# Performance work log

Hardware: AMD Instinct MI355X
Metric: run time of the kernel (lower is better)

## Reference

```python
import jax, jax.numpy as jnp
import numpy as np

DIM = 1024
HEADS = 16
DHEAD = 64
INNER = HEADS * DHEAD
EPS = 1e-5


def layer_norm(x, g, b):
    mu = jnp.mean(x, axis=-1, keepdims=True)
    var = jnp.mean(jnp.square(x - mu), axis=-1, keepdims=True)
    return (x - mu) * jax.lax.rsqrt(var + EPS) * g + b


def apply_rope(x, cos, sin):
    # x: [b, h, s, d]; cos/sin broadcast as [1, 1, s, d/2]
    d2 = x.shape[-1] // 2
    x1, x2 = x[..., :d2], x[..., d2:]
    return jnp.concatenate([x1 * cos - x2 * sin, x2 * cos + x1 * sin], axis=-1)


def setup_inputs() -> dict:
    key = jax.random.key(0)
    ks = jax.random.split(key, 10)
    B, N, S = 8, 256, 4096
    latents = jax.random.normal(ks[0], (B, N, DIM), dtype=jnp.float32)
    context = jax.random.normal(ks[1], (B, S, DIM), dtype=jnp.float32)
    cos = jax.random.uniform(ks[2], (S, DHEAD // 2), dtype=jnp.float32)
    sin = jax.random.uniform(ks[3], (S, DHEAD // 2), dtype=jnp.float32)
    init = lambda k, shp, fan_in: jax.random.normal(k, shp, dtype=jnp.float32) / np.sqrt(fan_in)
    return {
        "latents": latents,
        "context": context,
        "cos": cos,
        "sin": sin,
        "ln_lat_g": jnp.ones((DIM,), jnp.float32),
        "ln_lat_b": jnp.zeros((DIM,), jnp.float32),
        "ln_ctx_g": jnp.ones((DIM,), jnp.float32),
        "ln_ctx_b": jnp.zeros((DIM,), jnp.float32),
        "Wq": init(ks[4], (DIM, INNER), DIM),
        "Wkv": init(ks[5], (DIM, 2 * INNER), DIM),
        "Wo": init(ks[6], (INNER, DIM), INNER),
        "bo": jnp.zeros((DIM,), jnp.float32),
    }


def reference(latents, context, cos, sin, ln_lat_g, ln_lat_b, ln_ctx_g, ln_ctx_b, Wq, Wkv, Wo, bo):
    b, n, _ = latents.shape
    s = context.shape[1]
    lat = layer_norm(latents, ln_lat_g, ln_lat_b)
    ctx = layer_norm(context, ln_ctx_g, ln_ctx_b)
    q = (lat @ Wq).reshape(b, n, HEADS, DHEAD).transpose(0, 2, 1, 3)   # [b,h,n,d]
    kv = ctx @ Wkv
    k, v = jnp.split(kv, 2, axis=-1)
    k = k.reshape(b, s, HEADS, DHEAD).transpose(0, 2, 1, 3)           # [b,h,s,d]
    v = v.reshape(b, s, HEADS, DHEAD).transpose(0, 2, 1, 3)
    k = apply_rope(k, cos[None, None], sin[None, None])
    scale = DHEAD ** (-0.5)
    attn = jnp.einsum('bhnd,bhsd->bhns', q, k) * scale
    attn = jnp.clip(attn, -11.0, 11.0)
    attn = jax.nn.softmax(attn, axis=-1)
    out = jnp.einsum('bhns,bhsd->bhnd', attn, v)
    out = out.transpose(0, 2, 1, 3).reshape(b, n, INNER)
    return out @ Wo + bo
```

## Files before the change

### kernel.cpp

```cpp
#include <hip/hip_runtime.h>
#include <math.h>

#define DIM   1024
#define HEADS 16
#define DHEAD 64
#define NB    8
#define NLAT  256
#define SCTX  4096

typedef short bf16x8 __attribute__((ext_vector_type(8)));
typedef float f32x4  __attribute__((ext_vector_type(4)));

__device__ __forceinline__ unsigned short f2b(float f) {
    union { float f; unsigned u; } x; x.f = f;
    unsigned r = x.u + 0x7FFFu + ((x.u >> 16) & 1u);
    return (unsigned short)(r >> 16);
}

__global__ __launch_bounds__(256) void ln_bf16_all(
    const float* __restrict__ latents, const float* __restrict__ context,
    const float* __restrict__ g_lat, const float* __restrict__ b_lat,
    const float* __restrict__ g_ctx, const float* __restrict__ b_ctx,
    unsigned short* __restrict__ lat_b, unsigned short* __restrict__ ctx_b)
{
    int rb = blockIdx.x, t = threadIdx.x;
    const float* x; const float* g; const float* b; unsigned short* y; int r;
    if (rb < NB * NLAT) { x = latents; g = g_lat; b = b_lat; y = lat_b; r = rb; }
    else { x = context; g = g_ctx; b = b_ctx; y = ctx_b; r = rb - NB * NLAT; }

    float4 v = ((const float4*)(x + (size_t)r * DIM))[t];
    float s  = v.x + v.y + v.z + v.w;
    float sq = v.x * v.x + v.y * v.y + v.z * v.z + v.w * v.w;
    #pragma unroll
    for (int off = 32; off > 0; off >>= 1) {
        s  += __shfl_down(s, off);
        sq += __shfl_down(sq, off);
    }
    __shared__ float ls[4], lq[4], smu, srs;
    int wid = t >> 6, lane = t & 63;
    if (lane == 0) { ls[wid] = s; lq[wid] = sq; }
    __syncthreads();
    if (t == 0) {
        s  = ls[0] + ls[1] + ls[2] + ls[3];
        sq = lq[0] + lq[1] + lq[2] + lq[3];
        float m   = s * (1.0f / DIM);
        float var = sq * (1.0f / DIM) - m * m;
        smu = m;
        srs = rsqrtf(var + 1e-5f);
    }
    __syncthreads();
    float mu = smu, rs = srs;
    float4 gg = ((const float4*)g)[t];
    float4 bb = ((const float4*)b)[t];
    ushort4 o;
    o.x = f2b((v.x - mu) * rs * gg.x + bb.x);
    o.y = f2b((v.y - mu) * rs * gg.y + bb.y);
    o.z = f2b((v.z - mu) * rs * gg.z + bb.z);
    o.w = f2b((v.w - mu) * rs * gg.w + bb.w);
    ((ushort4*)(y + (size_t)r * DIM))[t] = o;
}

__global__ __launch_bounds__(256) void transpose_all(
    const float* __restrict__ Wq, const float* __restrict__ Wkv,
    const float* __restrict__ Wo,
    unsigned short* __restrict__ Wqb, unsigned short* __restrict__ Wkvb,
    unsigned short* __restrict__ Wob)
{
    __shared__ unsigned short tile[32][33];
    const float* W; unsigned short* Wt; int N, coloff = 0;
    switch (blockIdx.z) {
        case 0: W = Wq;  Wt = Wqb;  N = DIM;     break;
        case 1: W = Wkv; Wt = Wkvb; N = 2 * DIM; break;
        case 2: W = Wkv; Wt = Wkvb; N = 2 * DIM; coloff = DIM; break;
        default: W = Wo; Wt = Wob;  N = DIM;     break;
    }
    int n0 = blockIdx.x * 32 + coloff, k0 = blockIdx.y * 32;
    int tx = threadIdx.x & 31, ty = threadIdx.x >> 5;
    #pragma unroll
    for (int i = 0; i < 4; ++i) {
        int k = k0 + ty + i * 8;
        tile[tx][ty + i * 8] = f2b(W[(size_t)k * N + n0 + tx]);
    }
    __syncthreads();
    #pragma unroll
    for (int i = 0; i < 4; ++i) {
        int n = n0 + ty + i * 8;
        Wt[(size_t)n * DIM + k0 + tx] = tile[ty + i * 8][tx];
    }
}

__global__ __launch_bounds__(256, 2) void gemm_mfma(
    const unsigned short* __restrict__ A, const unsigned short* __restrict__ Bn,
    int K, const float* __restrict__ bias,
    const float* __restrict__ cosp, const float* __restrict__ sinp,
    float* __restrict__ outf,
    unsigned short* __restrict__ outk, unsigned short* __restrict__ outv,
    int mode, int ldc)
{
    __shared__ __align__(16) unsigned short As[128 * 32];
    __shared__ __align__(16) unsigned short Bs[128 * 32];
    int t = threadIdx.x;
    int wave = t >> 6, lane = t & 63;
    int g = blockIdx.x;
    int m_tile, n_tile;
    if (mode == 2) {
        int xcd = g & 7, j = g >> 3;
        n_tile = j & 15;
        m_tile = (xcd << 5) + (j >> 4);
    } else {
        n_tile = g & 7;
        m_tile = g >> 3;
    }
    int m_base = m_tile * 128, n_base = n_tile * 128;
    int wr = wave >> 1, wc = wave & 1;

    f32x4 zero = {0.f, 0.f, 0.f, 0.f};
    f32x4 acc[4][4];
    #pragma unroll
    for (int i = 0; i < 4; ++i)
        #pragma unroll
        for (int j = 0; j < 4; ++j) acc[i][j] = zero;

    int srow = lane >> 2;
    int scol = (lane & 3) * 8;
    const unsigned short* Ag = A  + (size_t)m_base * K;
    const unsigned short* Bg = Bn + (size_t)n_base * K;

    const unsigned short* a_lds = As + (wr * 64 + (lane & 15)) * 32 + (lane >> 4) * 8;
    const unsigned short* b_lds = Bs + (wc * 64 + (lane & 15)) * 32 + (lane >> 4) * 8;

    for (int k0 = 0; k0 < K; k0 += 32) {
        __syncthreads();
        #pragma unroll
        for (int i = 0; i < 2; ++i) {
            int row = i * 64 + wave * 16 + srow;
            __builtin_amdgcn_global_load_lds(
                (const __attribute__((address_space(1))) void*)(Ag + (size_t)row * K + k0 + scol),
                (__attribute__((address_space(3))) void*)(As + (size_t)(i * 64 + wave * 16) * 32 + lane * 8),
                16, 0, 0);
            __builtin_amdgcn_global_load_lds(
                (const __attribute__((address_space(1))) void*)(Bg + (size_t)row * K + k0 + scol),
                (__attribute__((address_space(3))) void*)(Bs + (size_t)(i * 64 + wave * 16) * 32 + lane * 8),
                16, 0, 0);
        }
        __syncthreads();
        bf16x8 af[4], bfr[4];
        #pragma unroll
        for (int i = 0; i < 4; ++i) {
            af[i]  = *(const bf16x8*)(a_lds + i * 16 * 32);
            bfr[i] = *(const bf16x8*)(b_lds + i * 16 * 32);
        }
        #pragma unroll
        for (int i = 0; i < 4; ++i)
            #pragma unroll
            for (int j = 0; j < 4; ++j)
                acc[i][j] = __builtin_amdgcn_mfma_f32_16x16x32_bf16(af[i], bfr[j], acc[i][j], 0, 0, 0);
    }

    int cl = lane & 15, rq = lane >> 4;
    if (mode == 2 && n_base >= DIM) {
        #pragma unroll
        for (int i = 0; i < 4; ++i) {
            int s0 = m_base + wr * 64 + i * 16 + rq * 4;
            int b  = s0 >> 12, s = s0 & 4095;
            #pragma unroll
            for (int j = 0; j < 4; ++j) {
                int n2 = n_base + wc * 64 + j * 16 + cl - DIM;
                int h = n2 >> 6, d = n2 & 63;
                ushort4 pk;
                pk.x = f2b(acc[i][j][0]); pk.y = f2b(acc[i][j][1]);
                pk.z = f2b(acc[i][j][2]); pk.w = f2b(acc[i][j][3]);
                *(ushort4*)(outv + (((size_t)(b * HEADS + h) * DHEAD + d) * SCTX) + s) = pk;
            }
        }
    } else if (mode == 2) {
        #pragma unroll
        for (int i = 0; i < 4; ++i) {
            #pragma unroll
            for (int r = 0; r < 4; ++r) {
                int m = m_base + wr * 64 + i * 16 + rq * 4 + r;
                int b = m >> 12, s = m & 4095;
                #pragma unroll
                for (int j = 0; j < 2; ++j) {
                    int n = n_base + wc * 64 + j * 16 + cl;
                    int h = n >> 6, d1 = n & 63;
                    float x1 = acc[i][j][r], x2 = acc[i][j + 2][r];
                    float c  = cosp[s * 32 + d1];
                    float sn = sinp[s * 32 + d1];
                    unsigned short* kr =
                        outk + (((size_t)(b * HEADS + h) * SCTX + s) * DHEAD) + d1;
                    kr[0]  = f2b(x1 * c - x2 * sn);
                    kr[32] = f2b(x2 * c + x1 * sn);
                }
            }
        }
    } else {
        #pragma unroll
        for (int i = 0; i < 4; ++i) {
            #pragma unroll
            for (int j = 0; j < 4; ++j) {
                #pragma unroll
                for (int r = 0; r < 4; ++r) {
                    int m = m_base + wr * 64 + i * 16 + rq * 4 + r;
                    int n = n_base + wc * 64 + j * 16 + cl;
                    float cv = acc[i][j][r];
                    if (mode == 0) {
                        outf[(size_t)m * ldc + n] = cv + bias[n];
                    } else {
                        int b = m >> 8, nn = m & 255;
                        int h = n >> 6, d = n & 63;
                        outk[(((size_t)(b * HEADS + h) * NLAT + nn) * DHEAD) + d] = f2b(cv);
                    }
                }
            }
        }
    }
}

__global__ __launch_bounds__(256, 4) void attn_mfma(
    const unsigned short* __restrict__ qb,
    const unsigned short* __restrict__ kb,
    const unsigned short* __restrict__ vtb,
    float* __restrict__ accp,
    float* __restrict__ lp)
{
    __shared__ __align__(16) unsigned short Ks[64 * 64];
    __shared__ __align__(16) unsigned short Vs[64 * 64];
    __shared__ __align__(16) unsigned short Ps[4 * 32 * 72];

    int t = threadIdx.x, w = t >> 6, l = t & 63;
    int bh = blockIdx.x >> 3;
    int qh = (blockIdx.x >> 2) & 1;
    int sh = blockIdx.x & 3;
    int quad = l >> 4, ln = l & 15;
    int q0 = qh * 128 + w * 32;

    bf16x8 qf[2][2];
    const unsigned short* qbase = qb + ((size_t)bh * NLAT + q0) * DHEAD;
    #pragma unroll
    for (int qsub = 0; qsub < 2; ++qsub)
        #pragma unroll
        for (int kc = 0; kc < 2; ++kc)
            qf[qsub][kc] = *(const bf16x8*)(qbase + (qsub * 16 + ln) * DHEAD + kc * 32 + quad * 8);

    f32x4 acc[2][4];
    #pragma unroll
    for (int i = 0; i < 2; ++i)
        #pragma unroll
        for (int j = 0; j < 4; ++j) acc[i][j] = (f32x4){0.f, 0.f, 0.f, 0.f};
    float lacc[2] = {0.f, 0.f};

    int srow = t >> 3;
    int schk = t & 7;
    const unsigned short* kgb = kb  + (size_t)bh * SCTX * DHEAD;
    const unsigned short* vgb = vtb + (size_t)bh * DHEAD * SCTX;
    unsigned short* Pw = Ps + w * 32 * 72;

    const int s_begin = sh * 1024;
    const int NT = 1024 / 64;

    uint4 kreg[2], vreg[2];
    #pragma unroll
    for (int i = 0; i < 2; ++i) {
        int row = srow + 32 * i;
        kreg[i] = *(const uint4*)(kgb + (size_t)(s_begin + row) * DHEAD + schk * 8);
        vreg[i] = *(const uint4*)(vgb + (size_t)row * SCTX + s_begin + schk * 8);
    }

    for (int it = 0; it < NT; ++it) {
        __syncthreads();
        #pragma unroll
        for (int i = 0; i < 2; ++i) {
            int row = srow + 32 * i;
            int cpos = schk ^ (row & 7);
            *(uint4*)(Ks + row * 64 + cpos * 8) = kreg[i];
            *(uint4*)(Vs + row * 64 + cpos * 8) = vreg[i];
        }
        __syncthreads();
        if (it + 1 < NT) {
            int s0n = s_begin + (it + 1) * 64;
            #pragma unroll
            for (int i = 0; i < 2; ++i) {
                int row = srow + 32 * i;
                kreg[i] = *(const uint4*)(kgb + (size_t)(s0n + row) * DHEAD + schk * 8);
                vreg[i] = *(const uint4*)(vgb + (size_t)row * SCTX + s0n + schk * 8);
            }
        }

        #pragma unroll
        for (int msub = 0; msub < 4; ++msub) {
            bf16x8 af[2];
            #pragma unroll
            for (int kc = 0; kc < 2; ++kc) {
                int sr = msub * 16 + ln;
                int ck = (4 * kc + quad) ^ (ln & 7);
                af[kc] = *(const bf16x8*)(Ks + sr * 64 + ck * 8);
            }
            #pragma unroll
            for (int nsub = 0; nsub < 2; ++nsub) {
                f32x4 c = {0.f, 0.f, 0.f, 0.f};
                c = __builtin_amdgcn_mfma_f32_16x16x32_bf16(af[0], qf[nsub][0], c, 0, 0, 0);
                c = __builtin_amdgcn_mfma_f32_16x16x32_bf16(af[1], qf[nsub][1], c, 0, 0, 0);
                ushort4 pk;
                #pragma unroll
                for (int r = 0; r < 4; ++r) {
                    float sc = fminf(fmaxf(c[r] * 0.125f, -11.f), 11.f);
                    float p  = __expf(sc - 11.f);
                    lacc[nsub] += p;
                    ((unsigned short*)&pk)[r] = f2b(p);
                }
                *(ushort4*)(Pw + (nsub * 16 + ln) * 72 + msub * 16 + quad * 4) = pk;
            }
        }
        #pragma unroll
        for (int kc = 0; kc < 2; ++kc) {
            bf16x8 pa[2];
            #pragma unroll
            for (int qsub = 0; qsub < 2; ++qsub)
                pa[qsub] = *(const bf16x8*)(Pw + (qsub * 16 + ln) * 72 + kc * 32 + quad * 8);
            #pragma unroll
            for (int dsub = 0; dsub < 4; ++dsub) {
                int dr = dsub * 16 + ln;
                int ck = (4 * kc + quad) ^ (ln & 7);
                bf16x8 vb = *(const bf16x8*)(Vs + dr * 64 + ck * 8);
                acc[0][dsub] = __builtin_amdgcn_mfma_f32_16x16x32_bf16(pa[0], vb, acc[0][dsub], 0, 0, 0);
                acc[1][dsub] = __builtin_amdgcn_mfma_f32_16x16x32_bf16(pa[1], vb, acc[1][dsub], 0, 0, 0);
            }
        }
    }

    float* accs = accp + (size_t)sh * (NB * HEADS * NLAT * DHEAD);
    float* ls   = lp   + (size_t)sh * (NB * HEADS * NLAT);

    #pragma unroll
    for (int nsub = 0; nsub < 2; ++nsub) {
        float v = lacc[nsub];
        v += __shfl_xor(v, 16);
        v += __shfl_xor(v, 32);
        if (l < 16)
            ls[bh * NLAT + q0 + nsub * 16 + l] = v;
    }
    #pragma unroll
    for (int qsub = 0; qsub < 2; ++qsub)
        #pragma unroll
        for (int dsub = 0; dsub < 4; ++dsub)
            #pragma unroll
            for (int r = 0; r < 4; ++r) {
                int qg = q0 + qsub * 16 + quad * 4 + r;
                int dg = dsub * 16 + ln;
                accs[((size_t)bh * NLAT + qg) * DHEAD + dg] = acc[qsub][dsub][r];
            }
}

__global__ __launch_bounds__(256) void attn_finalize(
    const float* __restrict__ accp, const float* __restrict__ lp,
    unsigned short* __restrict__ aob)
{
    const int ACC = NB * HEADS * NLAT * DHEAD;
    const int LSZ = NB * HEADS * NLAT;
    int idx = blockIdx.x * 256 + threadIdx.x;
    int d = idx & 63;
    int rest = idx >> 6;
    int n = rest & 255, bh = rest >> 8;
    int b = bh >> 4, h = bh & 15;
    float a = accp[idx] + accp[idx + ACC] + accp[idx + 2 * ACC] + accp[idx + 3 * ACC];
    float l = lp[rest] + lp[rest + LSZ] + lp[rest + 2 * LSZ] + lp[rest + 3 * LSZ];
    aob[(((size_t)b * NLAT + n) * HEADS + h) * DHEAD + d] = f2b(a / l);
}

extern "C" void kernel_launch(void* const* d_in, const int* in_sizes, int n_in,
                              void* d_out, int out_size, void* d_ws, size_t ws_size,
                              hipStream_t stream) {
    const float* latents  = (const float*)d_in[0];
    const float* context  = (const float*)d_in[1];
    const float* cosp     = (const float*)d_in[2];
    const float* sinp     = (const float*)d_in[3];
    const float* ln_lat_g = (const float*)d_in[4];
    const float* ln_lat_b = (const float*)d_in[5];
    const float* ln_ctx_g = (const float*)d_in[6];
    const float* ln_ctx_b = (const float*)d_in[7];
    const float* Wq  = (const float*)d_in[8];
    const float* Wkv = (const float*)d_in[9];
    const float* Wo  = (const float*)d_in[10];
    const float* bo  = (const float*)d_in[11];
    float* out = (float*)d_out;

    char* base = (char*)d_ws;
    unsigned short* lat_b = (unsigned short*)(base + 0);
    unsigned short* ctx_b = (unsigned short*)(base + 4194304);
    unsigned short* Wqb   = (unsigned short*)(base + 71303168);
    unsigned short* Wkvb  = (unsigned short*)(base + 73400320);
    unsigned short* Wob   = (unsigned short*)(base + 77594624);
    unsigned short* q_b   = (unsigned short*)(base + 79691776);
    unsigned short* k_b   = (unsigned short*)(base + 83886080);
    unsigned short* vT_b  = (unsigned short*)(base + 150994944);
    float*          accp  = (float*)(base + 218103808);
    float*          lp    = (float*)(base + 251658240);
    unsigned short* aob   = (unsigned short*)(base + 252182528);

    hipLaunchKernelGGL(ln_bf16_all, dim3(NB * NLAT + NB * SCTX), dim3(256), 0, stream,
                       latents, context, ln_lat_g, ln_lat_b, ln_ctx_g, ln_ctx_b,
                       lat_b, ctx_b);
    hipLaunchKernelGGL(transpose_all, dim3(32, 32, 4), dim3(256), 0, stream,
                       Wq, Wkv, Wo, Wqb, Wkvb, Wob);
    hipLaunchKernelGGL(gemm_mfma, dim3(128), dim3(256), 0, stream,
                       lat_b, Wqb, DIM, (const float*)nullptr,
                       (const float*)nullptr, (const float*)nullptr,
                       (float*)nullptr, q_b, (unsigned short*)nullptr, 1, 0);
    hipLaunchKernelGGL(gemm_mfma, dim3(4096), dim3(256), 0, stream,
                       ctx_b, Wkvb, DIM, (const float*)nullptr,
                       cosp, sinp,
                       (float*)nullptr, k_b, vT_b, 2, 0);
    hipLaunchKernelGGL(attn_mfma, dim3(NB * HEADS * 8), dim3(256), 0, stream,
                       q_b, k_b, vT_b, accp, lp);
    hipLaunchKernelGGL(attn_finalize, dim3(NB * HEADS * NLAT * DHEAD / 256), dim3(256), 0, stream,
                       accp, lp, aob);
    hipLaunchKernelGGL(gemm_mfma, dim3(128), dim3(256), 0, stream,
                       aob, Wob, DIM, bo,
                       (const float*)nullptr, (const float*)nullptr,
                       out, (unsigned short*)nullptr, (unsigned short*)nullptr, 0, DIM);
}
```

Baseline: 572.1 us.

## Merge prep kernels and Q/KV GEMMs, deepen GEMM K-tile with swizzled LDS

Combines layernorm and weight transpose/convert into a single launch, and folds the Q projection GEMM into the KV GEMM launch as extra blocks. The GEMM K-step doubles to 64 with an XOR-swizzled LDS layout to cut bank conflicts and halve the number of barriers per K. The attention kernel's launch bound drops from 4 to 2 blocks per CU, which loosens register limits but may lower occupancy. These changes aim to cut launch overhead and LDS stalls, at the cost of more LDS per GEMM block.

After: 522.0 us. -8.8%, faster.

```diff
diff --git a/kernel.cpp b/kernel.cpp
--- a/kernel.cpp
+++ b/kernel.cpp
@@ -17,102 +17,113 @@
     return (unsigned short)(r >> 16);
 }
 
-__global__ __launch_bounds__(256) void ln_bf16_all(
+#define LN_BLOCKS (NB * NLAT + NB * SCTX)
+__global__ __launch_bounds__(256) void prep_all(
     const float* __restrict__ latents, const float* __restrict__ context,
     const float* __restrict__ g_lat, const float* __restrict__ b_lat,
     const float* __restrict__ g_ctx, const float* __restrict__ b_ctx,
-    unsigned short* __restrict__ lat_b, unsigned short* __restrict__ ctx_b)
-{
-    int rb = blockIdx.x, t = threadIdx.x;
-    const float* x; const float* g; const float* b; unsigned short* y; int r;
-    if (rb < NB * NLAT) { x = latents; g = g_lat; b = b_lat; y = lat_b; r = rb; }
-    else { x = context; g = g_ctx; b = b_ctx; y = ctx_b; r = rb - NB * NLAT; }
-
-    float4 v = ((const float4*)(x + (size_t)r * DIM))[t];
-    float s  = v.x + v.y + v.z + v.w;
-    float sq = v.x * v.x + v.y * v.y + v.z * v.z + v.w * v.w;
-    #pragma unroll
-    for (int off = 32; off > 0; off >>= 1) {
-        s  += __shfl_down(s, off);
-        sq += __shfl_down(sq, off);
-    }
-    __shared__ float ls[4], lq[4], smu, srs;
-    int wid = t >> 6, lane = t & 63;
-    if (lane == 0) { ls[wid] = s; lq[wid] = sq; }
-    __syncthreads();
-    if (t == 0) {
-        s  = ls[0] + ls[1] + ls[2] + ls[3];
-        sq = lq[0] + lq[1] + lq[2] + lq[3];
-        float m   = s * (1.0f / DIM);
-        float var = sq * (1.0f / DIM) - m * m;
-        smu = m;
-        srs = rsqrtf(var + 1e-5f);
-    }
-    __syncthreads();
-    float mu = smu, rs = srs;
-    float4 gg = ((const float4*)g)[t];
-    float4 bb = ((const float4*)b)[t];
-    ushort4 o;
-    o.x = f2b((v.x - mu) * rs * gg.x + bb.x);
-    o.y = f2b((v.y - mu) * rs * gg.y + bb.y);
-    o.z = f2b((v.z - mu) * rs * gg.z + bb.z);
-    o.w = f2b((v.w - mu) * rs * gg.w + bb.w);
-    ((ushort4*)(y + (size_t)r * DIM))[t] = o;
-}
-
-__global__ __launch_bounds__(256) void transpose_all(
     const float* __restrict__ Wq, const float* __restrict__ Wkv,
     const float* __restrict__ Wo,
+    unsigned short* __restrict__ lat_b, unsigned short* __restrict__ ctx_b,
     unsigned short* __restrict__ Wqb, unsigned short* __restrict__ Wkvb,
     unsigned short* __restrict__ Wob)
 {
     __shared__ unsigned short tile[32][33];
-    const float* W; unsigned short* Wt; int N, coloff = 0;
-    switch (blockIdx.z) {
-        case 0: W = Wq;  Wt = Wqb;  N = DIM;     break;
-        case 1: W = Wkv; Wt = Wkvb; N = 2 * DIM; break;
-        case 2: W = Wkv; Wt = Wkvb; N = 2 * DIM; coloff = DIM; break;
-        default: W = Wo; Wt = Wob;  N = DIM;     break;
-    }
-    int n0 = blockIdx.x * 32 + coloff, k0 = blockIdx.y * 32;
-    int tx = threadIdx.x & 31, ty = threadIdx.x >> 5;
-    #pragma unroll
-    for (int i = 0; i < 4; ++i) {
-        int k = k0 + ty + i * 8;
-        tile[tx][ty + i * 8] = f2b(W[(size_t)k * N + n0 + tx]);
-    }
-    __syncthreads();
-    #pragma unroll
-    for (int i = 0; i < 4; ++i) {
-        int n = n0 + ty + i * 8;
-        Wt[(size_t)n * DIM + k0 + tx] = tile[ty + i * 8][tx];
+    int gb = blockIdx.x, t = threadIdx.x;
+    if (gb < LN_BLOCKS) {
+        const float* x; const float* g; const float* b; unsigned short* y; int r;
+        if (gb < NB * NLAT) { x = latents; g = g_lat; b = b_lat; y = lat_b; r = gb; }
+        else { x = context; g = g_ctx; b = b_ctx; y = ctx_b; r = gb - NB * NLAT; }
+        float* ls = (float*)tile;
+        float* lq = ls + 4;
+        float* st = ls + 8;
+        float4 v = ((const float4*)(x + (size_t)r * DIM))[t];
+        float s  = v.x + v.y + v.z + v.w;
+        float sq = v.x * v.x + v.y * v.y + v.z * v.z + v.w * v.w;
+        #pragma unroll
+        for (int off = 32; off > 0; off >>= 1) {
+            s  += __shfl_down(s, off);
+            sq += __shfl_down(sq, off);
+        }
+        int wid = t >> 6, lane = t & 63;
+        if (lane == 0) { ls[wid] = s; lq[wid] = sq; }
+        __syncthreads();
+        if (t == 0) {
+            s  = ls[0] + ls[1] + ls[2] + ls[3];
+            sq = lq[0] + lq[1] + lq[2] + lq[3];
+            float m   = s * (1.0f / DIM);
+            float var = sq * (1.0f / DIM) - m * m;
+            st[0] = m;
+            st[1] = rsqrtf(var + 1e-5f);
+        }
+        __syncthreads();
+        float mu = st[0], rs = st[1];
+        float4 gg = ((const float4*)g)[t];
+        float4 bb = ((const float4*)b)[t];
+        ushort4 o;
+        o.x = f2b((v.x - mu) * rs * gg.x + bb.x);
+        o.y = f2b((v.y - mu) * rs * gg.y + bb.y);
+        o.z = f2b((v.z - mu) * rs * gg.z + bb.z);
+        o.w = f2b((v.w - mu) * rs * gg.w + bb.w);
+        ((ushort4*)(y + (size_t)r * DIM))[t] = o;
+    } else {
+        int id = gb - LN_BLOCKS;
+        int z = id >> 10, y = (id >> 5) & 31, xb = id & 31;
+        const float* W; unsigned short* Wt; int N, coloff = 0;
+        switch (z) {
+            case 0: W = Wq;  Wt = Wqb;  N = DIM;     break;
+            case 1: W = Wkv; Wt = Wkvb; N = 2 * DIM; break;
+            case 2: W = Wkv; Wt = Wkvb; N = 2 * DIM; coloff = DIM; break;
+            default: W = Wo; Wt = Wob;  N = DIM;     break;
+        }
+        int n0 = xb * 32 + coloff, k0 = y * 32;
+        int tx = t & 31, ty = t >> 5;
+        #pragma unroll
+        for (int i = 0; i < 4; ++i) {
+            int k = k0 + ty + i * 8;
+            tile[tx][ty + i * 8] = f2b(W[(size_t)k * N + n0 + tx]);
+        }
+        __syncthreads();
+        #pragma unroll
+        for (int i = 0; i < 4; ++i) {
+            int n = n0 + ty + i * 8;
+            Wt[(size_t)n * DIM + k0 + tx] = tile[ty + i * 8][tx];
+        }
     }
 }
 
 __global__ __launch_bounds__(256, 2) void gemm_mfma(
     const unsigned short* __restrict__ A, const unsigned short* __restrict__ Bn,
+    const unsigned short* __restrict__ Aq, const unsigned short* __restrict__ Bq,
     int K, const float* __restrict__ bias,
     const float* __restrict__ cosp, const float* __restrict__ sinp,
     float* __restrict__ outf,
     unsigned short* __restrict__ outk, unsigned short* __restrict__ outv,
+    unsigned short* __restrict__ outq,
     int mode, int ldc)
 {
-    __shared__ __align__(16) unsigned short As[128 * 32];
-    __shared__ __align__(16) unsigned short Bs[128 * 32];
+    __shared__ __align__(16) unsigned short As[128 * 64];
+    __shared__ __align__(16) unsigned short Bs[128 * 64];
     int t = threadIdx.x;
     int wave = t >> 6, lane = t & 63;
     int g = blockIdx.x;
     int m_tile, n_tile;
     if (mode == 2) {
-        int xcd = g & 7, j = g >> 3;
-        n_tile = j & 15;
-        m_tile = (xcd << 5) + (j >> 4);
+        if (g >= 4096) {
+            g -= 4096; mode = 1;
+            A = Aq; Bn = Bq;
+            n_tile = g & 7; m_tile = g >> 3;
+        } else {
+            int xcd = g & 7, j = g >> 3;
+            n_tile = j & 15;
+            m_tile = (xcd << 5) + (j >> 4);
+        }
     } else {
-        n_tile = g & 7;
-        m_tile = g >> 3;
+        n_tile = g & 7; m_tile = g >> 3;
     }
     int m_base = m_tile * 128, n_base = n_tile * 128;
     int wr = wave >> 1, wc = wave & 1;
+    int quad = lane >> 4, ln = lane & 15;
 
     f32x4 zero = {0.f, 0.f, 0.f, 0.f};
     f32x4 acc[4][4];
@@ -121,43 +132,46 @@
         #pragma unroll
         for (int j = 0; j < 4; ++j) acc[i][j] = zero;
 
-    int srow = lane >> 2;
-    int scol = (lane & 3) * 8;
     const unsigned short* Ag = A  + (size_t)m_base * K;
     const unsigned short* Bg = Bn + (size_t)n_base * K;
 
-    const unsigned short* a_lds = As + (wr * 64 + (lane & 15)) * 32 + (lane >> 4) * 8;
-    const unsigned short* b_lds = Bs + (wc * 64 + (lane & 15)) * 32 + (lane >> 4) * 8;
-
-    for (int k0 = 0; k0 < K; k0 += 32) {
-        __syncthreads();
-        #pragma unroll
-        for (int i = 0; i < 2; ++i) {
-            int row = i * 64 + wave * 16 + srow;
+    int srow  = lane >> 3;
+    int schk  = ((lane & 7) ^ srow) * 8;
+
+    for (int k0 = 0; k0 < K; k0 += 64) {
+        __syncthreads();
+        #pragma unroll
+        for (int j = 0; j < 4; ++j) {
+            int grp = j * 4 + wave;
+            int row = grp * 8 + srow;
             __builtin_amdgcn_global_load_lds(
-                (const __attribute__((address_space(1))) void*)(Ag + (size_t)row * K + k0 + scol),
-                (__attribute__((address_space(3))) void*)(As + (size_t)(i * 64 + wave * 16) * 32 + lane * 8),
+                (const __attribute__((address_space(1))) void*)(Ag + (size_t)row * K + k0 + schk),
+                (__attribute__((address_space(3))) void*)(As + grp * 512 + lane * 8),
                 16, 0, 0);
             __builtin_amdgcn_global_load_lds(
-                (const __attribute__((address_space(1))) void*)(Bg + (size_t)row * K + k0 + scol),
-                (__attribute__((address_space(3))) void*)(Bs + (size_t)(i * 64 + wave * 16) * 32 + lane * 8),
+                (const __attribute__((address_space(1))) void*)(Bg + (size_t)row * K + k0 + schk),
+                (__attribute__((address_space(3))) void*)(Bs + grp * 512 + lane * 8),
                 16, 0, 0);
         }
         __syncthreads();
-        bf16x8 af[4], bfr[4];
-        #pragma unroll
-        for (int i = 0; i < 4; ++i) {
-            af[i]  = *(const bf16x8*)(a_lds + i * 16 * 32);
-            bfr[i] = *(const bf16x8*)(b_lds + i * 16 * 32);
-        }
-        #pragma unroll
-        for (int i = 0; i < 4; ++i)
-            #pragma unroll
-            for (int j = 0; j < 4; ++j)
-                acc[i][j] = __builtin_amdgcn_mfma_f32_16x16x32_bf16(af[i], bfr[j], acc[i][j], 0, 0, 0);
-    }
-
-    int cl = lane & 15, rq = lane >> 4;
+        #pragma unroll
+        for (int kk = 0; kk < 2; ++kk) {
+            bf16x8 af[4], bfr[4];
+            int slot = ((kk * 4 + quad) ^ (ln & 7)) * 8;
+            #pragma unroll
+            for (int i = 0; i < 4; ++i) {
+                af[i]  = *(const bf16x8*)(As + (wr * 64 + i * 16 + ln) * 64 + slot);
+                bfr[i] = *(const bf16x8*)(Bs + (wc * 64 + i * 16 + ln) * 64 + slot);
+            }
+            #pragma unroll
+            for (int i = 0; i < 4; ++i)
+                #pragma unroll
+                for (int j = 0; j < 4; ++j)
+                    acc[i][j] = __builtin_amdgcn_mfma_f32_16x16x32_bf16(af[i], bfr[j], acc[i][j], 0, 0, 0);
+        }
+    }
+
+    int cl = ln, rq = quad;
     if (mode == 2 && n_base >= DIM) {
         #pragma unroll
         for (int i = 0; i < 4; ++i) {
@@ -209,7 +223,7 @@
                     } else {
                         int b = m >> 8, nn = m & 255;
                         int h = n >> 6, d = n & 63;
-                        outk[(((size_t)(b * HEADS + h) * NLAT + nn) * DHEAD) + d] = f2b(cv);
+                        outq[(((size_t)(b * HEADS + h) * NLAT + nn) * DHEAD) + d] = f2b(cv);
                     }
                 }
             }
@@ -217,7 +231,7 @@
     }
 }
 
-__global__ __launch_bounds__(256, 4) void attn_mfma(
+__global__ __launch_bounds__(256, 2) void attn_mfma(
     const unsigned short* __restrict__ qb,
     const unsigned short* __restrict__ kb,
     const unsigned short* __restrict__ vtb,
@@ -398,25 +412,21 @@
     float*          lp    = (float*)(base + 251658240);
     unsigned short* aob   = (unsigned short*)(base + 252182528);
 
-    hipLaunchKernelGGL(ln_bf16_all, dim3(NB * NLAT + NB * SCTX), dim3(256), 0, stream,
+    hipLaunchKernelGGL(prep_all, dim3(LN_BLOCKS + 4096), dim3(256), 0, stream,
                        latents, context, ln_lat_g, ln_lat_b, ln_ctx_g, ln_ctx_b,
-                       lat_b, ctx_b);
-    hipLaunchKernelGGL(transpose_all, dim3(32, 32, 4), dim3(256), 0, stream,
-                       Wq, Wkv, Wo, Wqb, Wkvb, Wob);
-    hipLaunchKernelGGL(gemm_mfma, dim3(128), dim3(256), 0, stream,
-                       lat_b, Wqb, DIM, (const float*)nullptr,
-                       (const float*)nullptr, (const float*)nullptr,
-                       (float*)nullptr, q_b, (unsigned short*)nullptr, 1, 0);
-    hipLaunchKernelGGL(gemm_mfma, dim3(4096), dim3(256), 0, stream,
-                       ctx_b, Wkvb, DIM, (const float*)nullptr,
+                       Wq, Wkv, Wo, lat_b, ctx_b, Wqb, Wkvb, Wob);
+    hipLaunchKernelGGL(gemm_mfma, dim3(4096 + 128), dim3(256), 0, stream,
+                       ctx_b, Wkvb, lat_b, Wqb, DIM, (const float*)nullptr,
                        cosp, sinp,
-                       (float*)nullptr, k_b, vT_b, 2, 0);
+                       (float*)nullptr, k_b, vT_b, q_b, 2, 0);
     hipLaunchKernelGGL(attn_mfma, dim3(NB * HEADS * 8), dim3(256), 0, stream,
                        q_b, k_b, vT_b, accp, lp);
     hipLaunchKernelGGL(attn_finalize, dim3(NB * HEADS * NLAT * DHEAD / 256), dim3(256), 0, stream,
                        accp, lp, aob);
     hipLaunchKernelGGL(gemm_mfma, dim3(128), dim3(256), 0, stream,
-                       aob, Wob, DIM, bo,
+                       aob, Wob, (const unsigned short*)nullptr, (const unsigned short*)nullptr,
+                       DIM, bo,
                        (const float*)nullptr, (const float*)nullptr,
-                       out, (unsigned short*)nullptr, (unsigned short*)nullptr, 0, DIM);
-}
+                       out, (unsigned short*)nullptr, (unsigned short*)nullptr,
+                       (unsigned short*)nullptr, 0, DIM);
+}
```
